# Performance work log

Measured on AMD Instinct MI355X. Metric: run time of the kernel, lower is better.

The kernel has to match this reference:

```python
import jax, jax.numpy as jnp
import numpy as np

ON_OFF = "off"  # init kwarg: 'off' includes the next-frame temporal candidate

def setup_inputs() -> dict:
    key = jax.random.key(0)
    k1, k2 = jax.random.split(key)
    xs = jax.random.normal(k1, (4, 32, 128, 32), dtype=jnp.float32)  # [B,T,N,D]
    A = jax.random.randint(k2, (1, 128, 128), 0, 2, dtype=jnp.int32)  # [1,N,N] adjacency
    return {"xs": xs, "A": A}

def reference(xs, A):
    B, T, N, D = xs.shape
    # A_f = A + I ; neighbors are nonzero entries (self-loop included via eye)
    A_f = A[0].astype(xs.dtype) + jnp.eye(N, dtype=xs.dtype)
    spatial_mask = A_f != 0  # [N,N] : spatial_mask[n, j] -> j is neighbor of n

    # Candidate set per (frame t, node n): prev-frame self, next-frame self (on_off=='off'),
    # and all spatial neighbors at frame t. Padded to fixed size K = N + 2 with masks.
    spat = jnp.broadcast_to(xs[:, :, None, :, :], (B, T, N, N, D))   # [B,T,N,N,D]
    prev = jnp.concatenate([xs[:, :1], xs[:, :-1]], axis=1)          # [B,T,N,D] (t=0 masked)
    nxt = jnp.concatenate([xs[:, 1:], xs[:, -1:]], axis=1)           # [B,T,N,D] (t=T-1 masked)
    cand = jnp.concatenate([prev[:, :, :, None, :], nxt[:, :, :, None, :], spat], axis=3)  # [B,T,N,N+2,D]

    t = jnp.arange(T)
    prev_m = jnp.broadcast_to((t > 0)[:, None, None], (T, N, 1))
    if ON_OFF == "off":
        next_m = jnp.broadcast_to((t < T - 1)[:, None, None], (T, N, 1))
    else:
        next_m = jnp.zeros((T, N, 1), dtype=bool)
    sp_m = jnp.broadcast_to(spatial_mask[None], (T, N, N))
    mask = jnp.concatenate([prev_m, next_m, sp_m], axis=2)  # [T,N,N+2]

    # Masked median = torch.median semantics (lower median): sort with +inf padding,
    # pick index (k-1)//2 where k = number of valid candidates.
    vals = jnp.where(mask[None, :, :, :, None], cand, jnp.inf)
    vals = jnp.sort(vals, axis=3)
    k = mask.sum(axis=2)              # [T,N]
    med_idx = (k - 1) // 2            # lower median index
    idx = jnp.broadcast_to(med_idx[None, :, :, None, None], (B, T, N, 1, D))
    ys = jnp.take_along_axis(vals, idx, axis=3)[:, :, :, 0, :]  # [B,T,N,D]
    return ys
```

## Files before the change

kernel.cpp:

```cpp
#include <hip/hip_runtime.h>
#include <stdint.h>
#include <math.h>

#define BB 4
#define TT 32
#define NN 128
#define DD 32
#define NPB 16
#define TPB (NPB * DD)
#define NBLK (BB * TT * (NN / NPB))
#define CAP 16
#define NK (CAP + 2)

__device__ __forceinline__ int bin8(float x) {
    int i = (int)fmaf(x, 5.0f, 4.0f);
    i = i < 0 ? 0 : i;
    return i > 7 ? 7 : i;
}

__global__ __launch_bounds__(TPB) void median_kernel(const float* __restrict__ xs,
                                                     const int* __restrict__ A,
                                                     float* __restrict__ out) {
    __shared__ float sval[NN * DD];
    __shared__ uint8_t sbin[NN * DD];
    __shared__ __align__(16) uint32_t sbit[8 * DD * 4];
    __shared__ uint32_t snbr_w[NPB * NN / 4];
    __shared__ __align__(16) uint32_t smask[NPB][4];
    __shared__ int sdeg[NPB];

    const int tid = threadIdx.x;
    const int bid = blockIdx.x;
    const int g = ((bid & 7) << 7) | (bid >> 3);
    const int ng = g & (NN / NPB - 1);
    const int t  = (g >> 3) & (TT - 1);
    const int b  = g >> 8;
    const int n0 = ng * NPB;

    const int d = tid & (DD - 1);
    const int nl = tid >> 5;
    const int n = n0 + nl;
    const int pv = (t > 0) ? 1 : 0;
    const int nv = (t < TT - 1) ? 1 : 0;
    const int ne = pv + nv;

    float exv0 = 0.0f, exv1 = 0.0f;
    if (pv) exv0 = xs[(((size_t)(b * TT + t - 1) * NN) + n) * DD + d];
    if (nv) {
        float v = xs[(((size_t)(b * TT + t + 1) * NN) + n) * DD + d];
        if (pv) exv1 = v; else exv0 = v;
    }

    const float4* src4 = (const float4*)(xs + ((size_t)(b * TT + t) * NN) * DD);
    #pragma unroll
    for (int s = 0; s < 2; ++s) {
        int i4 = tid + (s << 9);
        float4 f = src4[i4];
        ((float4*)sval)[i4] = f;
        uint32_t pk = (uint32_t)bin8(f.x) | ((uint32_t)bin8(f.y) << 8)
                    | ((uint32_t)bin8(f.z) << 16) | ((uint32_t)bin8(f.w) << 24);
        ((uint32_t*)sbin)[i4] = pk;
    }

    {
        uint8_t* snbr = (uint8_t*)snbr_w;
        const int lane = tid & 63;
        const int wid = tid >> 6;
        const unsigned long long lmask = (1ULL << lane) - 1ULL;
        #pragma unroll
        for (int h = 0; h < 2; ++h) {
            const int rr = wid * 2 + h;
            const int nrow = n0 + rr;
            const int* arow = A + nrow * NN;
            const bool b0 = (arow[lane] != 0) || (lane == nrow);
            const bool b1 = (arow[lane + 64] != 0) || (lane + 64 == nrow);
            const unsigned long long m0 = __ballot(b0);
            const unsigned long long m1 = __ballot(b1);
            const int c0 = __popcll(m0);
            if (b0) snbr[rr * NN + __popcll(m0 & lmask)] = (uint8_t)lane;
            if (b1) snbr[rr * NN + c0 + __popcll(m1 & lmask)] = (uint8_t)(lane + 64);
            if (lane == 0) {
                sdeg[rr] = c0 + __popcll(m1);
                smask[rr][0] = (uint32_t)m0;
                smask[rr][1] = (uint32_t)(m0 >> 32);
                smask[rr][2] = (uint32_t)m1;
                smask[rr][3] = (uint32_t)(m1 >> 32);
            }
        }
    }
    __syncthreads();

    {
        const int rep = tid >> 7;
        const int wo  = (tid >> 5) & 3;
        const int dd  = tid & 31;
        const int ba = rep * 2, bc = ba + 1;
        uint32_t lo = 0u, hi = 0u;
        #pragma unroll 8
        for (int q = 0; q < 32; ++q) {
            const int bv = (int)sbin[(wo * 32 + q) * DD + dd];
            lo |= (bv == ba) ? (1u << q) : 0u;
            hi |= (bv == bc) ? (1u << q) : 0u;
        }
        sbit[ba * 128 + dd * 4 + wo] = lo;
        sbit[bc * 128 + dd * 4 + wo] = hi;
    }
    __syncthreads();

    const int dg = sdeg[nl];
    const int k = dg + ne;
    const uint32_t r = (uint32_t)((k - 1) >> 1);
    const uint8_t* nb = (const uint8_t*)snbr_w + nl * NN;
    const float INFV = __uint_as_float(0x7F800000u);
    const int be0 = bin8(exv0);
    const int be1 = bin8(exv1);

    const uint4 am4 = *((const uint4*)smask[nl]);
    int hist[8];
    const uint4* sbit4 = (const uint4*)sbit;
    #pragma unroll
    for (int bb = 0; bb < 8; ++bb) {
        uint4 w = sbit4[bb * 32 + d];
        hist[bb] = __popc(w.x & am4.x) + __popc(w.y & am4.y)
                 + __popc(w.z & am4.z) + __popc(w.w & am4.w);
    }

    uint32_t cum = 0, lowcnt = 0, mexp = 0;
    int selbin = -1;
    #pragma unroll
    for (int bb = 0; bb < 8; ++bb) {
        uint32_t bc = (uint32_t)hist[bb] + ((ne >= 1 && be0 == bb) ? 1u : 0u)
                                         + ((ne == 2 && be1 == bb) ? 1u : 0u);
        uint32_t nc = cum + bc;
        if (selbin < 0 && r < nc) { selbin = bb; lowcnt = cum; mexp = bc; }
        cum = nc;
    }
    const bool fb = (mexp > CAP);
    const uint32_t rp = r - lowcnt;

    const int sb = fb ? 0 : selbin;
    const uint4 wsel = sbit4[sb * 32 + d];
    unsigned long long bm0 = (((unsigned long long)(wsel.y & am4.y)) << 32) | (wsel.x & am4.x);
    unsigned long long bm1 = (((unsigned long long)(wsel.w & am4.w)) << 32) | (wsel.z & am4.z);
    const int mc_sp = fb ? 0 : (__popcll(bm0) + __popcll(bm1));
    int ids[CAP];
    #pragma unroll
    for (int u = 0; u < CAP; ++u) {
        const bool lo = (bm0 != 0ull);
        const unsigned long long mm_ = lo ? bm0 : bm1;
        const int ff = __ffsll((unsigned long long)mm_) - 1;
        ids[u] = (lo ? ff : 64 + ff) & 127;
        const unsigned long long cl = mm_ & (mm_ - 1ull);
        bm0 = lo ? cl : bm0;
        bm1 = lo ? bm1 : cl;
    }

    float ki[NK];
    #pragma unroll
    for (int u = 0; u < CAP; ++u)
        ki[u] = (u < mc_sp) ? sval[ids[u] * DD + d] : INFV;
    const bool t0 = (ne >= 1) && (be0 == selbin) && !fb;
    const bool t1 = (ne == 2) && (be1 == selbin) && !fb;
    ki[CAP]     = t0 ? exv0 : INFV;
    ki[CAP + 1] = t1 ? exv1 : INFV;

    uint32_t cn[NK];
    #pragma unroll
    for (int u = 0; u < NK; ++u) cn[u] = 0;
    #pragma unroll
    for (int u = 0; u < NK; ++u) {
        #pragma unroll
        for (int v = u + 1; v < NK; ++v) {
            const bool lt = ki[v] < ki[u];
            cn[u] += lt ? 1u : 0u;
            cn[v] += lt ? 0u : 1u;
        }
    }
    float result = 0.0f;
    #pragma unroll
    for (int u = 0; u < NK; ++u) {
        const bool valid = (u < CAP) ? (u < mc_sp) : ((u == CAP) ? t0 : t1);
        if (valid && cn[u] == rp) result = ki[u];
    }

    if (__ballot(fb)) {
        bool done = !fb;
        for (int i0 = 0; __ballot(!done && i0 < k); i0 += 8) {
            float k8[8]; uint32_t c8[8];
            #pragma unroll
            for (int u = 0; u < 8; ++u) {
                int i = i0 + u;
                float sv = sval[nb[i & 127] * DD + d];
                float ev = ((i - dg) == 0) ? exv0 : exv1;
                float v = (i < dg) ? sv : ev;
                k8[u] = (i < k) ? v : INFV;
                c8[u] = 0;
            }
            for (int j = 0; j < dg; ++j) {
                float xv = sval[nb[j] * DD + d];
                #pragma unroll
                for (int u = 0; u < 8; ++u) c8[u] += (xv < k8[u]);
            }
            if (ne >= 1) {
                #pragma unroll
                for (int u = 0; u < 8; ++u) c8[u] += (exv0 < k8[u]);
            }
            if (ne == 2) {
                #pragma unroll
                for (int u = 0; u < 8; ++u) c8[u] += (exv1 < k8[u]);
            }
            #pragma unroll
            for (int u = 0; u < 8; ++u) {
                if (!done && (i0 + u) < k && c8[u] == r) { result = k8[u]; done = true; }
            }
        }
        if (__ballot(!done)) {
            for (int i0 = 0; __ballot(!done && i0 < k); i0 += 4) {
                float k4[4]; uint32_t lt4[4], le4[4];
                #pragma unroll
                for (int u = 0; u < 4; ++u) {
                    int i = i0 + u;
                    float sv = sval[nb[i & 127] * DD + d];
                    float ev = ((i - dg) == 0) ? exv0 : exv1;
                    float v = (i < dg) ? sv : ev;
                    k4[u] = (i < k) ? v : INFV;
                    lt4[u] = 0; le4[u] = 0;
                }
                for (int j = 0; j < dg; ++j) {
                    float xv = sval[nb[j] * DD + d];
                    #pragma unroll
                    for (int u = 0; u < 4; ++u) { lt4[u] += (xv < k4[u]); le4[u] += (xv <= k4[u]); }
                }
                if (ne >= 1) {
                    #pragma unroll
                    for (int u = 0; u < 4; ++u) { lt4[u] += (exv0 < k4[u]); le4[u] += (exv0 <= k4[u]); }
                }
                if (ne == 2) {
                    #pragma unroll
                    for (int u = 0; u < 4; ++u) { lt4[u] += (exv1 < k4[u]); le4[u] += (exv1 <= k4[u]); }
                }
                #pragma unroll
                for (int u = 0; u < 4; ++u) {
                    if (!done && (i0 + u) < k && lt4[u] <= r && r < le4[u]) {
                        result = k4[u]; done = true;
                    }
                }
            }
        }
    }

    out[(((size_t)(b * TT + t) * NN) + n) * DD + d] = result;
}

extern "C" void kernel_launch(void* const* d_in, const int* in_sizes, int n_in,
                              void* d_out, int out_size, void* d_ws, size_t ws_size,
                              hipStream_t stream) {
    const float* xs = (const float*)d_in[0];
    const int* A = (const int*)d_in[1];
    float* out = (float*)d_out;
    (void)d_ws; (void)ws_size;

    median_kernel<<<NBLK, TPB, 0, stream>>>(xs, A, out);
}
```

Baseline: 110.1 us.

## Restrict overflow fallback to selected bin and drop neighbor list/bin arrays

When the selected histogram bin holds more than CAP candidates, the fallback now ranks only the candidates inside that bin, walking the bitmask, in a noinline helper. Before, it rank-counted over the full neighbor list. This removes the shared byte-bin array and the compacted neighbor index list. Bins are now recomputed from sval while the bitplanes are built, and the degree comes from the popcount of the adjacency mask. The aim is less shared memory, fewer stores during setup, and a cheaper, lower-register fallback. The cost is a divergent serial loop in the rare fallback and some extra ALU work for bin8.

```diff
diff --git a/kernel.cpp b/kernel.cpp
--- a/kernel.cpp
+++ b/kernel.cpp
@@ -18,15 +18,51 @@
     return i > 7 ? 7 : i;
 }
 
+__device__ __attribute__((noinline))
+float fb_band_median(const float* sval, int d,
+                     unsigned long long b0, unsigned long long b1,
+                     bool tb0, bool tb1, float e0, float e1, uint32_t rp) {
+    unsigned long long c0 = b0, c1 = b1;
+    bool u0 = tb0, u1 = tb1;
+    for (;;) {
+        float vi;
+        if (c0 | c1) {
+            const bool lo = (c0 != 0ull);
+            unsigned long long mm_ = lo ? c0 : c1;
+            const int ff = __ffsll(mm_) - 1;
+            const int id = lo ? ff : 64 + ff;
+            vi = sval[id * DD + d];
+            mm_ &= (mm_ - 1ull);
+            if (lo) c0 = mm_; else c1 = mm_;
+        } else if (u0) { vi = e0; u0 = false; }
+        else if (u1)   { vi = e1; u1 = false; }
+        else break;
+        uint32_t lt = 0, le = 0;
+        unsigned long long m0 = b0, m1 = b1;
+        while (m0 | m1) {
+            const bool lo = (m0 != 0ull);
+            unsigned long long mm_ = lo ? m0 : m1;
+            const int ff = __ffsll(mm_) - 1;
+            const int id = lo ? ff : 64 + ff;
+            const float x = sval[id * DD + d];
+            lt += (x < vi) ? 1u : 0u;
+            le += (x <= vi) ? 1u : 0u;
+            mm_ &= (mm_ - 1ull);
+            if (lo) m0 = mm_; else m1 = mm_;
+        }
+        if (tb0) { lt += (e0 < vi) ? 1u : 0u; le += (e0 <= vi) ? 1u : 0u; }
+        if (tb1) { lt += (e1 < vi) ? 1u : 0u; le += (e1 <= vi) ? 1u : 0u; }
+        if (lt <= rp && rp < le) return vi;
+    }
+    return 0.0f;
+}
+
 __global__ __launch_bounds__(TPB) void median_kernel(const float* __restrict__ xs,
                                                      const int* __restrict__ A,
                                                      float* __restrict__ out) {
-    __shared__ float sval[NN * DD];
-    __shared__ uint8_t sbin[NN * DD];
+    __shared__ __align__(16) float sval[NN * DD];
     __shared__ __align__(16) uint32_t sbit[8 * DD * 4];
-    __shared__ uint32_t snbr_w[NPB * NN / 4];
     __shared__ __align__(16) uint32_t smask[NPB][4];
-    __shared__ int sdeg[NPB];
 
     const int tid = threadIdx.x;
     const int bid = blockIdx.x;
@@ -54,18 +90,12 @@
     #pragma unroll
     for (int s = 0; s < 2; ++s) {
         int i4 = tid + (s << 9);
-        float4 f = src4[i4];
-        ((float4*)sval)[i4] = f;
-        uint32_t pk = (uint32_t)bin8(f.x) | ((uint32_t)bin8(f.y) << 8)
-                    | ((uint32_t)bin8(f.z) << 16) | ((uint32_t)bin8(f.w) << 24);
-        ((uint32_t*)sbin)[i4] = pk;
+        ((float4*)sval)[i4] = src4[i4];
     }
 
     {
-        uint8_t* snbr = (uint8_t*)snbr_w;
         const int lane = tid & 63;
         const int wid = tid >> 6;
-        const unsigned long long lmask = (1ULL << lane) - 1ULL;
         #pragma unroll
         for (int h = 0; h < 2; ++h) {
             const int rr = wid * 2 + h;
@@ -75,11 +105,7 @@
             const bool b1 = (arow[lane + 64] != 0) || (lane + 64 == nrow);
             const unsigned long long m0 = __ballot(b0);
             const unsigned long long m1 = __ballot(b1);
-            const int c0 = __popcll(m0);
-            if (b0) snbr[rr * NN + __popcll(m0 & lmask)] = (uint8_t)lane;
-            if (b1) snbr[rr * NN + c0 + __popcll(m1 & lmask)] = (uint8_t)(lane + 64);
             if (lane == 0) {
-                sdeg[rr] = c0 + __popcll(m1);
                 smask[rr][0] = (uint32_t)m0;
                 smask[rr][1] = (uint32_t)(m0 >> 32);
                 smask[rr][2] = (uint32_t)m1;
@@ -97,7 +123,7 @@
         uint32_t lo = 0u, hi = 0u;
         #pragma unroll 8
         for (int q = 0; q < 32; ++q) {
-            const int bv = (int)sbin[(wo * 32 + q) * DD + dd];
+            const int bv = bin8(sval[(wo * 32 + q) * DD + dd]);
             lo |= (bv == ba) ? (1u << q) : 0u;
             hi |= (bv == bc) ? (1u << q) : 0u;
         }
@@ -106,15 +132,16 @@
     }
     __syncthreads();
 
-    const int dg = sdeg[nl];
+    const uint4 am4 = *((const uint4*)smask[nl]);
+    const unsigned long long am0 = (((unsigned long long)am4.y) << 32) | am4.x;
+    const unsigned long long am1 = (((unsigned long long)am4.w) << 32) | am4.z;
+    const int dg = __popcll(am0) + __popcll(am1);
     const int k = dg + ne;
     const uint32_t r = (uint32_t)((k - 1) >> 1);
-    const uint8_t* nb = (const uint8_t*)snbr_w + nl * NN;
     const float INFV = __uint_as_float(0x7F800000u);
     const int be0 = bin8(exv0);
     const int be1 = bin8(exv1);
 
-    const uint4 am4 = *((const uint4*)smask[nl]);
     int hist[8];
     const uint4* sbit4 = (const uint4*)sbit;
     #pragma unroll
@@ -136,119 +163,59 @@
     }
     const bool fb = (mexp > CAP);
     const uint32_t rp = r - lowcnt;
-
-    const int sb = fb ? 0 : selbin;
-    const uint4 wsel = sbit4[sb * 32 + d];
+    const bool tb0 = (ne >= 1) && (be0 == selbin);
+    const bool tb1 = (ne == 2) && (be1 == selbin);
+
+    const uint4 wsel = sbit4[selbin * 32 + d];
     unsigned long long bm0 = (((unsigned long long)(wsel.y & am4.y)) << 32) | (wsel.x & am4.x);
     unsigned long long bm1 = (((unsigned long long)(wsel.w & am4.w)) << 32) | (wsel.z & am4.z);
     const int mc_sp = fb ? 0 : (__popcll(bm0) + __popcll(bm1));
-    int ids[CAP];
-    #pragma unroll
-    for (int u = 0; u < CAP; ++u) {
-        const bool lo = (bm0 != 0ull);
-        const unsigned long long mm_ = lo ? bm0 : bm1;
-        const int ff = __ffsll((unsigned long long)mm_) - 1;
-        ids[u] = (lo ? ff : 64 + ff) & 127;
-        const unsigned long long cl = mm_ & (mm_ - 1ull);
-        bm0 = lo ? cl : bm0;
-        bm1 = lo ? bm1 : cl;
-    }
-
-    float ki[NK];
-    #pragma unroll
-    for (int u = 0; u < CAP; ++u)
-        ki[u] = (u < mc_sp) ? sval[ids[u] * DD + d] : INFV;
-    const bool t0 = (ne >= 1) && (be0 == selbin) && !fb;
-    const bool t1 = (ne == 2) && (be1 == selbin) && !fb;
-    ki[CAP]     = t0 ? exv0 : INFV;
-    ki[CAP + 1] = t1 ? exv1 : INFV;
-
-    uint32_t cn[NK];
-    #pragma unroll
-    for (int u = 0; u < NK; ++u) cn[u] = 0;
-    #pragma unroll
-    for (int u = 0; u < NK; ++u) {
-        #pragma unroll
-        for (int v = u + 1; v < NK; ++v) {
-            const bool lt = ki[v] < ki[u];
-            cn[u] += lt ? 1u : 0u;
-            cn[v] += lt ? 0u : 1u;
-        }
-    }
-    float result = 0.0f;
-    #pragma unroll
-    for (int u = 0; u < NK; ++u) {
-        const bool valid = (u < CAP) ? (u < mc_sp) : ((u == CAP) ? t0 : t1);
-        if (valid && cn[u] == rp) result = ki[u];
-    }
-
-    if (__ballot(fb)) {
-        bool done = !fb;
-        for (int i0 = 0; __ballot(!done && i0 < k); i0 += 8) {
-            float k8[8]; uint32_t c8[8];
+    {
+        unsigned long long c0 = bm0, c1 = bm1;
+        int ids[CAP];
+        #pragma unroll
+        for (int u = 0; u < CAP; ++u) {
+            const bool lo = (c0 != 0ull);
+            const unsigned long long mm_ = lo ? c0 : c1;
+            const int ff = __ffsll(mm_) - 1;
+            ids[u] = (lo ? ff : 64 + ff) & 127;
+            const unsigned long long cl = mm_ & (mm_ - 1ull);
+            c0 = lo ? cl : c0;
+            c1 = lo ? c1 : cl;
+        }
+
+        float ki[NK];
+        #pragma unroll
+        for (int u = 0; u < CAP; ++u)
+            ki[u] = (u < mc_sp) ? sval[ids[u] * DD + d] : INFV;
+        const bool t0 = tb0 && !fb;
+        const bool t1 = tb1 && !fb;
+        ki[CAP]     = t0 ? exv0 : INFV;
+        ki[CAP + 1] = t1 ? exv1 : INFV;
+
+        uint32_t cn[NK];
+        #pragma unroll
+        for (int u = 0; u < NK; ++u) cn[u] = 0;
+        #pragma unroll
+        for (int u = 0; u < NK; ++u) {
             #pragma unroll
-            for (int u = 0; u < 8; ++u) {
-                int i = i0 + u;
-                float sv = sval[nb[i & 127] * DD + d];
-                float ev = ((i - dg) == 0) ? exv0 : exv1;
-                float v = (i < dg) ? sv : ev;
-                k8[u] = (i < k) ? v : INFV;
-                c8[u] = 0;
+            for (int v = u + 1; v < NK; ++v) {
+                const bool lt = ki[v] < ki[u];
+                cn[u] += lt ? 1u : 0u;
+                cn[v] += lt ? 0u : 1u;
             }
-            for (int j = 0; j < dg; ++j) {
-                float xv = sval[nb[j] * DD + d];
-                #pragma unroll
-                for (int u = 0; u < 8; ++u) c8[u] += (xv < k8[u]);
-            }
-            if (ne >= 1) {
-                #pragma unroll
-                for (int u = 0; u < 8; ++u) c8[u] += (exv0 < k8[u]);
-            }
-            if (ne == 2) {
-                #pragma unroll
-                for (int u = 0; u < 8; ++u) c8[u] += (exv1 < k8[u]);
-            }
-            #pragma unroll
-            for (int u = 0; u < 8; ++u) {
-                if (!done && (i0 + u) < k && c8[u] == r) { result = k8[u]; done = true; }
-            }
-        }
-        if (__ballot(!done)) {
-            for (int i0 = 0; __ballot(!done && i0 < k); i0 += 4) {
-                float k4[4]; uint32_t lt4[4], le4[4];
-                #pragma unroll
-                for (int u = 0; u < 4; ++u) {
-                    int i = i0 + u;
-                    float sv = sval[nb[i & 127] * DD + d];
-                    float ev = ((i - dg) == 0) ? exv0 : exv1;
-                    float v = (i < dg) ? sv : ev;
-                    k4[u] = (i < k) ? v : INFV;
-                    lt4[u] = 0; le4[u] = 0;
-                }
-                for (int j = 0; j < dg; ++j) {
-                    float xv = sval[nb[j] * DD + d];
-                    #pragma unroll
-                    for (int u = 0; u < 4; ++u) { lt4[u] += (xv < k4[u]); le4[u] += (xv <= k4[u]); }
-                }
-                if (ne >= 1) {
-                    #pragma unroll
-                    for (int u = 0; u < 4; ++u) { lt4[u] += (exv0 < k4[u]); le4[u] += (exv0 <= k4[u]); }
-                }
-                if (ne == 2) {
-                    #pragma unroll
-                    for (int u = 0; u < 4; ++u) { lt4[u] += (exv1 < k4[u]); le4[u] += (exv1 <= k4[u]); }
-                }
-                #pragma unroll
-                for (int u = 0; u < 4; ++u) {
-                    if (!done && (i0 + u) < k && lt4[u] <= r && r < le4[u]) {
-                        result = k4[u]; done = true;
-                    }
-                }
-            }
-        }
-    }
-
-    out[(((size_t)(b * TT + t) * NN) + n) * DD + d] = result;
+        }
+        float result = 0.0f;
+        #pragma unroll
+        for (int u = 0; u < NK; ++u) {
+            const bool valid = (u < CAP) ? (u < mc_sp) : ((u == CAP) ? t0 : t1);
+            if (valid && cn[u] == rp) result = ki[u];
+        }
+
+        if (fb) result = fb_band_median(sval, d, bm0, bm1, tb0, tb1, exv0, exv1, rp);
+
+        out[(((size_t)(b * TT + t) * NN) + n) * DD + d] = result;
+    }
 }
 
 extern "C" void kernel_launch(void* const* d_in, const int* in_sizes, int n_in,
```

Measured after the change: 224.0 us. 2.04x slower.
